# Kernel optimization log

Hardware: AMD Instinct MI355X
Metric: run time of the kernel (lower is better)

Reference implementation:

```python
import jax, jax.numpy as jnp
import numpy as np

NEG_INF = -1.0e9
LEAKY_SLOPE = 0.2


def setup_inputs() -> dict:
    key = jax.random.key(0)
    k1, k2, k3, k4, k5 = jax.random.split(key, 5)
    B, N, F_in, H, D = 4, 2048, 128, 4, 32
    x = jax.random.normal(k1, (B, N, F_in), dtype=jnp.float32)
    # binary adjacency; force self-loops so every row has >=1 neighbour
    adj = jax.random.randint(k2, (N, N), 0, 2).astype(jnp.float32)
    adj = jnp.maximum(adj, jnp.eye(N, dtype=jnp.float32))
    W = jax.random.normal(k3, (H, F_in, D), dtype=jnp.float32) * (1.0 / np.sqrt(F_in))
    a_left = jax.random.normal(k4, (H, D, 1), dtype=jnp.float32) * (1.0 / np.sqrt(D))
    a_right = jax.random.normal(k5, (H, D, 1), dtype=jnp.float32) * (1.0 / np.sqrt(D))
    bias = jnp.zeros((H, D), dtype=jnp.float32)
    return {"x": x, "adj": adj, "W": W, "a_left": a_left, "a_right": a_right, "bias": bias}


def reference(x, adj, W, a_left, a_right, bias):
    # x: (B,N,F) ; W: (H,F,D) -> h: (B,H,N,D)
    h = jnp.einsum('bnf,hfd->bhnd', x, W)
    # separable additive scores: (B,H,N)
    al = jnp.einsum('bhnd,hd->bhn', h, a_left[..., 0])
    ar = jnp.einsum('bhnd,hd->bhn', h, a_right[..., 0])
    e = al[:, :, :, None] + ar[:, :, None, :]          # (B,H,N,N)
    e = jnp.where(e >= 0, e, LEAKY_SLOPE * e)           # LeakyReLU(0.2)
    mask = adj[None, None] > 0.5
    e = jnp.where(mask, e, NEG_INF)
    alpha = jax.nn.softmax(e, axis=-1)                  # (B,H,N,N)
    # inference: dropout on alpha is identity
    out = jnp.einsum('bhmn,bhnd->bhmd', alpha, h) + bias[None, :, None, :]
    out = jax.nn.elu(out)
    # concat heads: (B,H,N,D) -> (B,N,H*D)
    B, H, N, D = out.shape
    out = jnp.transpose(out, (0, 2, 1, 3)).reshape(B, N, H * D)
    return out
```

## Files before the change

### kernel.cpp

```cpp
#include <hip/hip_runtime.h>
#include <hip/hip_bf16.h>

#define Bn 4
#define Nn 2048
#define Fn 128
#define Hn 4
#define Dn 32
#define LOG2E 1.44269504f

typedef __attribute__((ext_vector_type(4))) float f32x4;
typedef __attribute__((ext_vector_type(8))) short s16x8;
typedef __attribute__((ext_vector_type(4))) short s16x4;
typedef _Float16 f16x8 __attribute__((ext_vector_type(8)));

__device__ __forceinline__ short f2h(float f) {
  _Float16 h = (_Float16)f;
  return __builtin_bit_cast(short, h);
}

__global__ __launch_bounds__(128) void k_proj(
    const float* __restrict__ x, const float* __restrict__ W,
    const float* __restrict__ aL, const float* __restrict__ aR,
    float* __restrict__ al, float* __restrict__ ar, short* __restrict__ ht)
{
  __shared__ float xl[4 * Fn];
  const int blk = blockIdx.x;
  const int b = blk >> 9;
  const int n0 = (blk & 511) * 4;
  const int t = threadIdx.x;

  const f32x4* xg = (const f32x4*)(x + ((size_t)b * Nn + n0) * Fn);
  ((f32x4*)xl)[t] = xg[t];
  __syncthreads();

  const int head = t >> 5, d = t & 31;
  const float* Wp = W + head * Fn * Dn + d;
  float acc[4] = {0.f, 0.f, 0.f, 0.f};
  const f32x4* xl4 = (const f32x4*)xl;
  #pragma unroll 4
  for (int f4 = 0; f4 < Fn / 4; ++f4) {
    const float w0 = Wp[(f4 * 4 + 0) * Dn];
    const float w1 = Wp[(f4 * 4 + 1) * Dn];
    const float w2 = Wp[(f4 * 4 + 2) * Dn];
    const float w3 = Wp[(f4 * 4 + 3) * Dn];
    #pragma unroll
    for (int r = 0; r < 4; ++r) {
      const f32x4 xv = xl4[r * 32 + f4];
      acc[r] = fmaf(xv[0], w0, acc[r]);
      acc[r] = fmaf(xv[1], w1, acc[r]);
      acc[r] = fmaf(xv[2], w2, acc[r]);
      acc[r] = fmaf(xv[3], w3, acc[r]);
    }
  }

  const int bh = b * Hn + head;
  const float aLv = aL[head * Dn + d];
  const float aRv = aR[head * Dn + d];
  #pragma unroll
  for (int r = 0; r < 4; ++r) {
    float vl = acc[r] * aLv;
    float vr = acc[r] * aRv;
    #pragma unroll
    for (int m = 1; m < 32; m <<= 1) {
      vl += __shfl_xor(vl, m);
      vr += __shfl_xor(vr, m);
    }
    if (d == 0) {
      al[bh * Nn + n0 + r] = vl * LOG2E;
      ar[bh * Nn + n0 + r] = vr * LOG2E;
    }
  }

  s16x4 hv;
  #pragma unroll
  for (int r = 0; r < 4; ++r) hv[r] = f2h(acc[r]);
  *(s16x4*)(ht + ((size_t)bh * Dn + d) * Nn + n0) = hv;
}

__global__ __launch_bounds__(256) void k_attn(
    const float* __restrict__ adj, const float* __restrict__ al, const float* __restrict__ ar,
    const short* __restrict__ ht, const float* __restrict__ bias, float* __restrict__ out)
{
  __shared__ float accS[4][16][32];
  __shared__ float lS[4][16];

  const int blk = blockIdx.x;
  const int mt = blk & 127, bh = blk >> 7;
  const int b = bh >> 2, head = bh & 3;
  const int m0 = mt * 16;
  const int t = threadIdx.x;
  const int wv = t >> 6, lane = t & 63;
  const int r = lane & 15, g = lane >> 4;

  const float al_m = al[bh * Nn + m0 + r];
  const float* arp  = ar  + bh * Nn;
  const float* adjp = adj + (size_t)(m0 + r) * Nn;
  const short* htA = ht + ((size_t)bh * Dn + r) * Nn;
  const short* htB = htA + 16 * Nn;

  float ps = 0.f;
  f32x4 accA = {0.f,0.f,0.f,0.f}, accB = {0.f,0.f,0.f,0.f};

  for (int ci = 0; ci < 16; ++ci) {
    const int nb = wv * 512 + ci * 32 + g * 8;
    const f32x4 ar0 = *(const f32x4*)(arp + nb);
    const f32x4 ar1 = *(const f32x4*)(arp + nb + 4);
    const f32x4 aj0 = *(const f32x4*)(adjp + nb);
    const f32x4 aj1 = *(const f32x4*)(adjp + nb + 4);

    float p[8];
    #pragma unroll
    for (int j = 0; j < 4; ++j) {
      float s0 = al_m + ar0[j];
      float s1 = al_m + ar1[j];
      s0 = fmaxf(s0, 0.2f * s0) - 4.0f;
      s1 = fmaxf(s1, 0.2f * s1) - 4.0f;
      const float e0 = exp2f(s0);
      const float e1 = exp2f(s1);
      p[j]     = aj0[j] > 0.5f ? e0 : 0.0f;
      p[j + 4] = aj1[j] > 0.5f ? e1 : 0.0f;
    }

    #pragma unroll
    for (int j = 0; j < 8; ++j) ps += p[j];

    f16x8 pf;
    #pragma unroll
    for (int j = 0; j < 8; ++j) pf[j] = (_Float16)p[j];
    const f16x8 hfA = __builtin_bit_cast(f16x8, *(const s16x8*)(htA + nb));
    const f16x8 hfB = __builtin_bit_cast(f16x8, *(const s16x8*)(htB + nb));
    accA = __builtin_amdgcn_mfma_f32_16x16x32_f16(pf, hfA, accA, 0, 0, 0);
    accB = __builtin_amdgcn_mfma_f32_16x16x32_f16(pf, hfB, accB, 0, 0, 0);
  }

  ps += __shfl_xor(ps, 16);
  ps += __shfl_xor(ps, 32);

  #pragma unroll
  for (int q = 0; q < 4; ++q) {
    accS[wv][4 * g + q][r]      = accA[q];
    accS[wv][4 * g + q][r + 16] = accB[q];
  }
  if (g == 0) lS[wv][r] = ps;
  __syncthreads();

  const int row = t >> 4, dc = t & 15;
  const float L = lS[0][row] + lS[1][row] + lS[2][row] + lS[3][row];
  const float inv = 1.f / L;
  #pragma unroll
  for (int hh = 0; hh < 2; ++hh) {
    const int dcol = dc + 16 * hh;
    float v = accS[0][row][dcol] + accS[1][row][dcol]
            + accS[2][row][dcol] + accS[3][row][dcol];
    v = v * inv + bias[head * Dn + dcol];
    v = v > 0.f ? v : __expf(v) - 1.f;
    out[((size_t)b * Nn + m0 + row) * (Hn * Dn) + head * Dn + dcol] = v;
  }
}

extern "C" void kernel_launch(void* const* d_in, const int* in_sizes, int n_in,
                              void* d_out, int out_size, void* d_ws, size_t ws_size,
                              hipStream_t stream) {
  const float* x    = (const float*)d_in[0];
  const float* adj  = (const float*)d_in[1];
  const float* W    = (const float*)d_in[2];
  const float* aL   = (const float*)d_in[3];
  const float* aR   = (const float*)d_in[4];
  const float* bias = (const float*)d_in[5];
  float* out = (float*)d_out;

  float* al = (float*)d_ws;
  float* ar = al + (Bn * Hn) * Nn;
  short* ht = (short*)(ar + (Bn * Hn) * Nn);

  hipLaunchKernelGGL(k_proj, dim3((Bn * Nn) / 4), dim3(128), 0, stream,
                     x, W, aL, aR, al, ar, ht);
  hipLaunchKernelGGL(k_attn, dim3((Bn * Hn) * (Nn / 16)), dim3(256), 0, stream,
                     adj, al, ar, ht, bias, out);
}
```

Baseline: 148.1 us.

## Pack adjacency to bitmask, MFMA projection, and widen attention blocks with LDS ar

Adds a pack kernel that turns the float adjacency into 64-bit ballot bitmasks and converts W to transposed fp16. The projection is rewritten to use MFMA on fp16-converted x. The attention kernel now uses 512 threads, stages ar in LDS, preloads all h fragments up front, and reads mask bits instead of floats. The aim is to cut the 16 MB adjacency re-read per head and batch down to a compact bitmask, at the cost of an extra launch and fp16 rounding of x and W in the projection.

Measured after the change: 122.6 us. 17.2% less time.

```diff
diff --git a/kernel.cpp b/kernel.cpp
--- a/kernel.cpp
+++ b/kernel.cpp
@@ -18,71 +18,112 @@
   return __builtin_bit_cast(short, h);
 }
 
-__global__ __launch_bounds__(128) void k_proj(
-    const float* __restrict__ x, const float* __restrict__ W,
+__global__ __launch_bounds__(256) void k_pack(
+    const float* __restrict__ adj, const float* __restrict__ W,
+    unsigned long long* __restrict__ adjbits, short* __restrict__ Wt)
+{
+  const int blk = blockIdx.x;
+  const int t = threadIdx.x;
+  if (blk < Nn) {
+    const int wv = t >> 6, lane = t & 63;
+    const float* ap = adj + (size_t)blk * Nn;
+    #pragma unroll
+    for (int s = 0; s < 8; ++s) {
+      const int n0 = (wv * 8 + s) * 64;
+      const unsigned long long m = __ballot(ap[n0 + lane] > 0.5f);
+      if (lane == 0) adjbits[blk * 32 + wv * 8 + s] = m;
+    }
+  } else {
+    const int h = blk - Nn;
+    const float* Wp = W + h * Fn * Dn;
+    #pragma unroll
+    for (int i = 0; i < 16; i += 4) {
+      const int idx = t * 16 + i;
+      const f32x4 w4 = *(const f32x4*)(Wp + idx);
+      const int k = idx >> 5, d0 = idx & 31;
+      #pragma unroll
+      for (int j = 0; j < 4; ++j)
+        Wt[(h * Dn + d0 + j) * Fn + k] = f2h(w4[j]);
+    }
+  }
+}
+
+__global__ __launch_bounds__(64) void k_proj(
+    const float* __restrict__ x, const short* __restrict__ Wt,
     const float* __restrict__ aL, const float* __restrict__ aR,
     float* __restrict__ al, float* __restrict__ ar, short* __restrict__ ht)
 {
-  __shared__ float xl[4 * Fn];
-  const int blk = blockIdx.x;
-  const int b = blk >> 9;
-  const int n0 = (blk & 511) * 4;
-  const int t = threadIdx.x;
-
-  const f32x4* xg = (const f32x4*)(x + ((size_t)b * Nn + n0) * Fn);
-  ((f32x4*)xl)[t] = xg[t];
-  __syncthreads();
-
-  const int head = t >> 5, d = t & 31;
-  const float* Wp = W + head * Fn * Dn + d;
-  float acc[4] = {0.f, 0.f, 0.f, 0.f};
-  const f32x4* xl4 = (const f32x4*)xl;
-  #pragma unroll 4
-  for (int f4 = 0; f4 < Fn / 4; ++f4) {
-    const float w0 = Wp[(f4 * 4 + 0) * Dn];
-    const float w1 = Wp[(f4 * 4 + 1) * Dn];
-    const float w2 = Wp[(f4 * 4 + 2) * Dn];
-    const float w3 = Wp[(f4 * 4 + 3) * Dn];
-    #pragma unroll
-    for (int r = 0; r < 4; ++r) {
-      const f32x4 xv = xl4[r * 32 + f4];
-      acc[r] = fmaf(xv[0], w0, acc[r]);
-      acc[r] = fmaf(xv[1], w1, acc[r]);
-      acc[r] = fmaf(xv[2], w2, acc[r]);
-      acc[r] = fmaf(xv[3], w3, acc[r]);
-    }
-  }
-
-  const int bh = b * Hn + head;
-  const float aLv = aL[head * Dn + d];
-  const float aRv = aR[head * Dn + d];
-  #pragma unroll
-  for (int r = 0; r < 4; ++r) {
-    float vl = acc[r] * aLv;
-    float vr = acc[r] * aRv;
-    #pragma unroll
-    for (int m = 1; m < 32; m <<= 1) {
-      vl += __shfl_xor(vl, m);
-      vr += __shfl_xor(vr, m);
-    }
-    if (d == 0) {
-      al[bh * Nn + n0 + r] = vl * LOG2E;
-      ar[bh * Nn + n0 + r] = vr * LOG2E;
-    }
-  }
-
-  s16x4 hv;
-  #pragma unroll
-  for (int r = 0; r < 4; ++r) hv[r] = f2h(acc[r]);
-  *(s16x4*)(ht + ((size_t)bh * Dn + d) * Nn + n0) = hv;
-}
-
-__global__ __launch_bounds__(256) void k_attn(
-    const float* __restrict__ adj, const float* __restrict__ al, const float* __restrict__ ar,
-    const short* __restrict__ ht, const float* __restrict__ bias, float* __restrict__ out)
+  const int m0 = blockIdx.x * 16;
+  const int b = m0 >> 11, nloc = m0 & 2047;
+  const int lane = threadIdx.x;
+  const int r = lane & 15, g = lane >> 4;
+
+  const float* xp = x + (size_t)(m0 + r) * Fn + g * 8;
+  f32x4 c[8] = {};
+  #pragma unroll
+  for (int ks = 0; ks < 4; ++ks) {
+    const f32x4 xa = *(const f32x4*)(xp + ks * 32);
+    const f32x4 xb = *(const f32x4*)(xp + ks * 32 + 4);
+    f16x8 af;
+    #pragma unroll
+    for (int j = 0; j < 4; ++j) { af[j] = (_Float16)xa[j]; af[j + 4] = (_Float16)xb[j]; }
+    const short* wp = Wt + r * Fn + ks * 32 + g * 8;
+    #pragma unroll
+    for (int cf = 0; cf < 8; ++cf) {
+      const f16x8 bf = __builtin_bit_cast(f16x8, *(const s16x8*)(wp + cf * 16 * Fn));
+      c[cf] = __builtin_amdgcn_mfma_f32_16x16x32_f16(af, bf, c[cf], 0, 0, 0);
+    }
+  }
+
+  float vl[16] = {}, vr[16] = {};
+  #pragma unroll
+  for (int cf = 0; cf < 8; ++cf) {
+    const int hh = cf >> 1;
+    const float aLv = aL[hh * Dn + (cf & 1) * 16 + r] * LOG2E;
+    const float aRv = aR[hh * Dn + (cf & 1) * 16 + r] * LOG2E;
+    #pragma unroll
+    for (int q = 0; q < 4; ++q) {
+      vl[hh * 4 + q] = fmaf(c[cf][q], aLv, vl[hh * 4 + q]);
+      vr[hh * 4 + q] = fmaf(c[cf][q], aRv, vr[hh * 4 + q]);
+    }
+  }
+  #pragma unroll
+  for (int i = 0; i < 16; ++i) {
+    #pragma unroll
+    for (int st = 1; st < 16; st <<= 1) {
+      vl[i] += __shfl_xor(vl[i], st);
+      vr[i] += __shfl_xor(vr[i], st);
+    }
+  }
+  float ol = vl[0], orr = vr[0];
+  #pragma unroll
+  for (int i = 1; i < 16; ++i) {
+    ol  = (r == i) ? vl[i] : ol;
+    orr = (r == i) ? vr[i] : orr;
+  }
+  const int hh = r >> 2, qq = r & 3;
+  al[(size_t)(b * Hn + hh) * Nn + nloc + g * 4 + qq] = ol;
+  ar[(size_t)(b * Hn + hh) * Nn + nloc + g * 4 + qq] = orr;
+
+  #pragma unroll
+  for (int cf = 0; cf < 8; ++cf) {
+    const int hd = cf >> 1, d = (cf & 1) * 16 + r;
+    s16x4 hv;
+    #pragma unroll
+    for (int q = 0; q < 4; ++q) hv[q] = f2h(c[cf][q]);
+    *(s16x4*)(ht + ((size_t)(b * Hn + hd) * Dn + d) * Nn + nloc + g * 4) = hv;
+  }
+}
+
+__global__ __launch_bounds__(512, 4) void k_attn(
+    const unsigned long long* __restrict__ adjbits,
+    const float* __restrict__ al, const float* __restrict__ ar,
+    const short* __restrict__ ht, const float* __restrict__ bias,
+    float* __restrict__ out)
 {
-  __shared__ float accS[4][16][32];
-  __shared__ float lS[4][16];
+  __shared__ float ar_s[Nn];
+  __shared__ float accS[8][16][32];
+  __shared__ float lS[8][16];
 
   const int blk = blockIdx.x;
   const int mt = blk & 127, bh = blk >> 7;
@@ -92,46 +133,57 @@
   const int wv = t >> 6, lane = t & 63;
   const int r = lane & 15, g = lane >> 4;
 
-  const float al_m = al[bh * Nn + m0 + r];
-  const float* arp  = ar  + bh * Nn;
-  const float* adjp = adj + (size_t)(m0 + r) * Nn;
-  const short* htA = ht + ((size_t)bh * Dn + r) * Nn;
+  ((f32x4*)ar_s)[t] = ((const f32x4*)(ar + (size_t)bh * Nn))[t];
+
+  const unsigned long long abits = adjbits[(size_t)(m0 + r) * 32 + wv * 4 + g];
+  const float al_m = al[(size_t)bh * Nn + m0 + r] - 4.0f;
+
+  const short* htA = ht + ((size_t)bh * Dn + r) * Nn + wv * 256 + g * 64;
   const short* htB = htA + 16 * Nn;
-
+  s16x8 hA0 = *(const s16x8*)(htA);      s16x8 hB0 = *(const s16x8*)(htB);
+  s16x8 hA1 = *(const s16x8*)(htA + 8);  s16x8 hB1 = *(const s16x8*)(htB + 8);
+  s16x8 hA2 = *(const s16x8*)(htA + 16); s16x8 hB2 = *(const s16x8*)(htB + 16);
+  s16x8 hA3 = *(const s16x8*)(htA + 24); s16x8 hB3 = *(const s16x8*)(htB + 24);
+  s16x8 hA4 = *(const s16x8*)(htA + 32); s16x8 hB4 = *(const s16x8*)(htB + 32);
+  s16x8 hA5 = *(const s16x8*)(htA + 40); s16x8 hB5 = *(const s16x8*)(htB + 40);
+  s16x8 hA6 = *(const s16x8*)(htA + 48); s16x8 hB6 = *(const s16x8*)(htB + 48);
+  s16x8 hA7 = *(const s16x8*)(htA + 56); s16x8 hB7 = *(const s16x8*)(htB + 56);
+
+  __syncthreads();
+
+  const float* arp = ar_s + wv * 256 + g * 64;
   float ps = 0.f;
   f32x4 accA = {0.f,0.f,0.f,0.f}, accB = {0.f,0.f,0.f,0.f};
 
-  for (int ci = 0; ci < 16; ++ci) {
-    const int nb = wv * 512 + ci * 32 + g * 8;
-    const f32x4 ar0 = *(const f32x4*)(arp + nb);
-    const f32x4 ar1 = *(const f32x4*)(arp + nb + 4);
-    const f32x4 aj0 = *(const f32x4*)(adjp + nb);
-    const f32x4 aj1 = *(const f32x4*)(adjp + nb + 4);
-
-    float p[8];
-    #pragma unroll
-    for (int j = 0; j < 4; ++j) {
-      float s0 = al_m + ar0[j];
-      float s1 = al_m + ar1[j];
-      s0 = fmaxf(s0, 0.2f * s0) - 4.0f;
-      s1 = fmaxf(s1, 0.2f * s1) - 4.0f;
-      const float e0 = exp2f(s0);
-      const float e1 = exp2f(s1);
-      p[j]     = aj0[j] > 0.5f ? e0 : 0.0f;
-      p[j + 4] = aj1[j] > 0.5f ? e1 : 0.0f;
-    }
-
-    #pragma unroll
-    for (int j = 0; j < 8; ++j) ps += p[j];
-
-    f16x8 pf;
-    #pragma unroll
-    for (int j = 0; j < 8; ++j) pf[j] = (_Float16)p[j];
-    const f16x8 hfA = __builtin_bit_cast(f16x8, *(const s16x8*)(htA + nb));
-    const f16x8 hfB = __builtin_bit_cast(f16x8, *(const s16x8*)(htB + nb));
-    accA = __builtin_amdgcn_mfma_f32_16x16x32_f16(pf, hfA, accA, 0, 0, 0);
-    accB = __builtin_amdgcn_mfma_f32_16x16x32_f16(pf, hfB, accB, 0, 0, 0);
-  }
+  #define CHUNK(ci, hAx, hBx)                                                  \
+  {                                                                            \
+    const f32x4 a0 = *(const f32x4*)(arp + ci * 8);                            \
+    const f32x4 a1 = *(const f32x4*)(arp + ci * 8 + 4);                        \
+    const unsigned int byte = (unsigned int)(abits >> (ci * 8)) & 0xffu;       \
+    float p[8];                                                                \
+    _Pragma("unroll")                                                          \
+    for (int j = 0; j < 4; ++j) {                                              \
+      const float s0 = al_m + a0[j];                                           \
+      const float s1 = al_m + a1[j];                                           \
+      const float e0 = exp2f(fmaxf(s0, fmaf(0.2f, s0, -3.2f)));                \
+      const float e1 = exp2f(fmaxf(s1, fmaf(0.2f, s1, -3.2f)));                \
+      p[j]     = (byte & (1u << j))       ? e0 : 0.f;                          \
+      p[j + 4] = (byte & (1u << (j + 4))) ? e1 : 0.f;                          \
+    }                                                                          \
+    _Pragma("unroll")                                                          \
+    for (int j = 0; j < 8; ++j) ps += p[j];                                    \
+    f16x8 pf;                                                                  \
+    _Pragma("unroll")                                                          \
+    for (int j = 0; j < 8; ++j) pf[j] = (_Float16)p[j];                        \
+    accA = __builtin_amdgcn_mfma_f32_16x16x32_f16(                             \
+        pf, __builtin_bit_cast(f16x8, hAx), accA, 0, 0, 0);                    \
+    accB = __builtin_amdgcn_mfma_f32_16x16x32_f16(                             \
+        pf, __builtin_bit_cast(f16x8, hBx), accB, 0, 0, 0);                    \
+  }
+
+  CHUNK(0, hA0, hB0) CHUNK(1, hA1, hB1) CHUNK(2, hA2, hB2) CHUNK(3, hA3, hB3)
+  CHUNK(4, hA4, hB4) CHUNK(5, hA5, hB5) CHUNK(6, hA6, hB6) CHUNK(7, hA7, hB7)
+  #undef CHUNK
 
   ps += __shfl_xor(ps, 16);
   ps += __shfl_xor(ps, 32);
@@ -144,18 +196,13 @@
   if (g == 0) lS[wv][r] = ps;
   __syncthreads();
 
-  const int row = t >> 4, dc = t & 15;
-  const float L = lS[0][row] + lS[1][row] + lS[2][row] + lS[3][row];
-  const float inv = 1.f / L;
-  #pragma unroll
-  for (int hh = 0; hh < 2; ++hh) {
-    const int dcol = dc + 16 * hh;
-    float v = accS[0][row][dcol] + accS[1][row][dcol]
-            + accS[2][row][dcol] + accS[3][row][dcol];
-    v = v * inv + bias[head * Dn + dcol];
-    v = v > 0.f ? v : __expf(v) - 1.f;
-    out[((size_t)b * Nn + m0 + row) * (Hn * Dn) + head * Dn + dcol] = v;
-  }
+  const int row = t >> 5, dc = t & 31;
+  float L = 0.f, v = 0.f;
+  #pragma unroll
+  for (int w = 0; w < 8; ++w) { L += lS[w][row]; v += accS[w][row][dc]; }
+  v = v / L + bias[head * Dn + dc];
+  v = v > 0.f ? v : __expf(v) - 1.f;
+  out[((size_t)b * Nn + m0 + row) * (Hn * Dn) + head * Dn + dc] = v;
 }
 
 extern "C" void kernel_launch(void* const* d_in, const int* in_sizes, int n_in,
@@ -172,9 +219,13 @@
   float* al = (float*)d_ws;
   float* ar = al + (Bn * Hn) * Nn;
   short* ht = (short*)(ar + (Bn * Hn) * Nn);
-
-  hipLaunchKernelGGL(k_proj, dim3((Bn * Nn) / 4), dim3(128), 0, stream,
-                     x, W, aL, aR, al, ar, ht);
-  hipLaunchKernelGGL(k_attn, dim3((Bn * Hn) * (Nn / 16)), dim3(256), 0, stream,
-                     adj, al, ar, ht, bias, out);
-}
+  unsigned long long* adjbits =
+      (unsigned long long*)(ht + (size_t)(Bn * Hn) * Dn * Nn);
+  short* Wt = (short*)(adjbits + Nn * (Nn / 64));
+
+  hipLaunchKernelGGL(k_pack, dim3(Nn + Hn), dim3(256), 0, stream, adj, W, adjbits, Wt);
+  hipLaunchKernelGGL(k_proj, dim3((Bn * Nn) / 16), dim3(64), 0, stream,
+                     x, Wt, aL, aR, al, ar, ht);
+  hipLaunchKernelGGL(k_attn, dim3((Bn * Hn) * (Nn / 16)), dim3(512), 0, stream,
+                     adjbits, al, ar, ht, bias, out);
+}
```
